# Performance work log

Hardware: AMD Instinct MI355X
Metric: run time of the kernel (lower is better)

Reference implementation:

```python
import jax, jax.numpy as jnp
import numpy as np


def setup_inputs() -> dict:
    key = jax.random.key(0)
    k1, k2, k3 = jax.random.split(key, 3)
    N, E, D_IN, D_OUT = 100000, 1600000, 64, 64
    x = jax.random.normal(k1, (N, D_IN), dtype=jnp.float32)
    edge_index = jax.random.randint(k2, (2, E), 0, N, dtype=jnp.int64)
    # Glorot-style init for the GCN weight, zero bias (PyG defaults)
    W = jax.random.normal(k3, (D_IN, D_OUT), dtype=jnp.float32) * (1.0 / np.sqrt(D_IN))
    b = jnp.zeros((D_OUT,), dtype=jnp.float32)
    return {"x": x, "edge_index": edge_index, "W": W, "b": b}


def reference(x, edge_index, W, b):
    # GCNConv (PyG semantics, add_self_loops=True, normalize=True) followed by
    # Dropout (eval mode -> identity) and ReLU.
    N = x.shape[0]
    # Linear transform first (small GEMM)
    xw = x @ W  # [N, D_OUT]
    # Add self-loops
    loops = jnp.arange(N, dtype=edge_index.dtype)
    row = jnp.concatenate([edge_index[0], loops])  # source nodes
    col = jnp.concatenate([edge_index[1], loops])  # destination nodes
    # Symmetric degree normalization: deg over destination index (PyG gcn_norm)
    ones = jnp.ones(col.shape[0], dtype=xw.dtype)
    deg = jax.ops.segment_sum(ones, col, num_segments=N)
    deg_inv_sqrt = jnp.where(deg > 0, jax.lax.rsqrt(deg), 0.0)
    norm = deg_inv_sqrt[row] * deg_inv_sqrt[col]  # [E+N]
    # Gather source features, scale, scatter-add to destinations
    msgs = norm[:, None] * xw[row]  # [E+N, D_OUT]
    out = jax.ops.segment_sum(msgs, col, num_segments=N)
    out = out + b
    # dropout in eval mode is identity
    return jax.nn.relu(out)
```

## Files before the change

### kernel.cpp

```cpp
#include <hip/hip_runtime.h>
#include <hip/hip_fp16.h>


#define D 64
#define BW 256
#define CAP 6144
#define EPT 16
#define PART_T 256
#define EPB (PART_T * EPT)

typedef __attribute__((ext_vector_type(8))) short bf16x8;
typedef __attribute__((ext_vector_type(4))) float f32x4;

__device__ __forceinline__ unsigned short f2bf(float f) {
    unsigned u = __float_as_uint(f);
    u += 0x7FFFu + ((u >> 16) & 1u);
    return (unsigned short)(u >> 16);
}

__global__ void k_part(const int* __restrict__ row, const int* __restrict__ col,
                       int* __restrict__ gcur, int* __restrict__ packed,
                       int E, int NBUCK) {
    extern __shared__ int sh[];
    int* lh   = sh;
    int* base = sh + NBUCK;
    for (int i = threadIdx.x; i < NBUCK; i += PART_T) lh[i] = 0;
    __syncthreads();
    int e0 = blockIdx.x * EPB + threadIdx.x;
    int rr[EPT], cc[EPT], pp[EPT];
#pragma unroll
    for (int i = 0; i < EPT; ++i) {
        int e = e0 + i * PART_T;
        if (e < E) {
            cc[i] = col[e];
            rr[i] = row[e];
            pp[i] = atomicAdd(&lh[cc[i] >> 8], 1);
        } else {
            cc[i] = -1;
        }
    }
    __syncthreads();
    int rot = (int)((blockIdx.x * 97u) % (unsigned)NBUCK);
    for (int j = threadIdx.x; j < NBUCK; j += PART_T) {
        int bu = j + rot; if (bu >= NBUCK) bu -= NBUCK;
        int h = lh[bu];
        if (h > 0) base[bu] = atomicAdd(&gcur[bu * 32], h);
    }
    __syncthreads();
#pragma unroll
    for (int i = 0; i < EPT; ++i) {
        if (cc[i] >= 0) {
            int bu = cc[i] >> 8;
            int pos = base[bu] + pp[i];
            if (pos < CAP)
                packed[(size_t)bu * CAP + pos] = (rr[i] << 8) | (cc[i] & 255);
        }
    }
}

__global__ void k_dis(const int* __restrict__ gcur, const int* __restrict__ packed,
                      float* __restrict__ dis, int N) {
    __shared__ int lh[BW];
    int b = blockIdx.x;
    lh[threadIdx.x] = 0;
    __syncthreads();
    int sz = min(gcur[b * 32], CAP);
    const int* pk = packed + (size_t)b * CAP;
    for (int i = threadIdx.x; i < sz; i += BW)
        atomicAdd(&lh[pk[i] & 255], 1);
    __syncthreads();
    int n = b * BW + threadIdx.x;
    if (n < N) dis[n] = rsqrtf((float)(lh[threadIdx.x] + 1));
}

__global__ __launch_bounds__(256, 4)
void k_gemm_mfma(const float* __restrict__ x, const float* __restrict__ W,
                 const float* __restrict__ dis, unsigned short* __restrict__ xw_h,
                 int N) {
    __shared__ float Ws[64 * 64];
    int tid = threadIdx.x;
    for (int i = tid; i < 4096; i += 256) Ws[i] = W[i];
    __syncthreads();
    int lane = tid & 63, wv = tid >> 6;
    int m = lane & 15, quad = lane >> 4;
    bf16x8 Bf[4][2];
#pragma unroll
    for (int t = 0; t < 4; ++t)
#pragma unroll
        for (int s = 0; s < 2; ++s) {
            bf16x8 f;
#pragma unroll
            for (int j = 0; j < 8; ++j)
                f[j] = (short)f2bf(Ws[(s * 32 + quad * 8 + j) * 64 + t * 16 + m]);
            Bf[t][s] = f;
        }
    int mt = blockIdx.x * 4 + wv;
    int row0 = mt * 16;
    if (row0 >= N) return;
    const float* xr = x + (size_t)(row0 + m) * 64 + quad * 8;
    float4 a0 = *(const float4*)(xr);
    float4 a1 = *(const float4*)(xr + 4);
    float4 a2 = *(const float4*)(xr + 32);
    float4 a3 = *(const float4*)(xr + 36);
    bf16x8 A0, A1;
    A0[0] = (short)f2bf(a0.x); A0[1] = (short)f2bf(a0.y);
    A0[2] = (short)f2bf(a0.z); A0[3] = (short)f2bf(a0.w);
    A0[4] = (short)f2bf(a1.x); A0[5] = (short)f2bf(a1.y);
    A0[6] = (short)f2bf(a1.z); A0[7] = (short)f2bf(a1.w);
    A1[0] = (short)f2bf(a2.x); A1[1] = (short)f2bf(a2.y);
    A1[2] = (short)f2bf(a2.z); A1[3] = (short)f2bf(a2.w);
    A1[4] = (short)f2bf(a3.x); A1[5] = (short)f2bf(a3.y);
    A1[6] = (short)f2bf(a3.z); A1[7] = (short)f2bf(a3.w);
    f32x4 acc[4];
#pragma unroll
    for (int t = 0; t < 4; ++t) {
        acc[t] = (f32x4){0.f, 0.f, 0.f, 0.f};
        acc[t] = __builtin_amdgcn_mfma_f32_16x16x32_bf16(A0, Bf[t][0], acc[t], 0, 0, 0);
        acc[t] = __builtin_amdgcn_mfma_f32_16x16x32_bf16(A1, Bf[t][1], acc[t], 0, 0, 0);
    }
    float4 dv = *(const float4*)(dis + row0 + quad * 4);
    float dsc[4] = {dv.x, dv.y, dv.z, dv.w};
#pragma unroll
    for (int t = 0; t < 4; ++t)
#pragma unroll
        for (int r = 0; r < 4; ++r) {
            int grow = row0 + quad * 4 + r;
            int gcol = t * 16 + m;
            xw_h[(size_t)grow * 64 + gcol] =
                __half_as_ushort(__float2half(acc[t][r] * dsc[r]));
        }
}

__global__ __launch_bounds__(1024, 8)
void k_gather(const int* __restrict__ gcur, const int* __restrict__ packed,
              const uint2* __restrict__ xwh, const float* __restrict__ bias,
              float4* __restrict__ out4, int N) {
    __shared__ int lh[BW], stt[BW], cur[BW];
    __shared__ int srtL[CAP];
    __shared__ int wsum[4];
    int b = blockIdx.x;
    int tid = threadIdx.x;
    if (tid < BW) lh[tid] = 0;
    __syncthreads();
    int sz = min(gcur[b * 32], CAP);
    const int* pk = packed + (size_t)b * CAP;
    for (int i = tid; i < sz; i += 1024)
        atomicAdd(&lh[pk[i] & 255], 1);
    __syncthreads();
    int lane = tid & 63, wv4 = tid >> 6;
    int v = (tid < BW) ? lh[tid] : 0;
    int s = v;
#pragma unroll
    for (int off = 1; off < 64; off <<= 1) {
        int u = __shfl_up(s, off);
        if (lane >= off) s += u;
    }
    if (tid < BW && lane == 63) wsum[wv4] = s;
    __syncthreads();
    if (tid < BW) {
        int woff = 0;
        for (int w = 0; w < 4; ++w) woff += (w < wv4) ? wsum[w] : 0;
        int st = woff + s - v;
        stt[tid] = st;
        cur[tid] = st;
    }
    __syncthreads();
    for (int i = tid; i < sz; i += 1024) {
        int p = pk[i];
        int pos = atomicAdd(&cur[p & 255], 1);
        srtL[pos] = p >> 8;
    }
    __syncthreads();
    int wv = tid >> 6;
    int q = lane >> 4;
    int l = lane & 15;
    const float4 bb = ((const float4*)bias)[l];
#define ADDV(h)                                                     \
    {                                                               \
        __half2 h0 = *(__half2*)&(h).x, h1 = *(__half2*)&(h).y;     \
        float2 f0 = __half22float2(h0), f1 = __half22float2(h1);    \
        acc.x += f0.x; acc.y += f0.y; acc.z += f1.x; acc.w += f1.y; \
    }
    for (int nn = wv * 16; nn < wv * 16 + 16; ++nn) {
        int node = b * BW + nn;
        if (node >= N) break;
        int k = lh[nn], s0 = stt[nn];
        float4 acc = make_float4(0.f, 0.f, 0.f, 0.f);
        if (q == 0) { uint2 hs = xwh[(size_t)node * 16 + l]; ADDV(hs); }
        int j = q;
        for (; j + 12 < k; j += 16) {
            int r0 = srtL[s0 + j];
            int r1 = srtL[s0 + j + 4];
            int r2 = srtL[s0 + j + 8];
            int r3 = srtL[s0 + j + 12];
            uint2 va = xwh[(size_t)r0 * 16 + l];
            uint2 vb = xwh[(size_t)r1 * 16 + l];
            uint2 vc = xwh[(size_t)r2 * 16 + l];
            uint2 vd = xwh[(size_t)r3 * 16 + l];
            ADDV(va); ADDV(vb); ADDV(vc); ADDV(vd);
        }
        for (; j < k; j += 4) { uint2 ve = xwh[(size_t)srtL[s0 + j] * 16 + l]; ADDV(ve); }
#pragma unroll
        for (int mm = 16; mm < 64; mm <<= 1) {
            acc.x += __shfl_xor(acc.x, mm);
            acc.y += __shfl_xor(acc.y, mm);
            acc.z += __shfl_xor(acc.z, mm);
            acc.w += __shfl_xor(acc.w, mm);
        }
        if (q == 0) {
            float dn = rsqrtf((float)(k + 1));
            float4 o;
            o.x = fmaxf(fmaf(dn, acc.x, bb.x), 0.f);
            o.y = fmaxf(fmaf(dn, acc.y, bb.y), 0.f);
            o.z = fmaxf(fmaf(dn, acc.z, bb.z), 0.f);
            o.w = fmaxf(fmaf(dn, acc.w, bb.w), 0.f);
            out4[(size_t)node * 16 + l] = o;
        }
    }
#undef ADDV
}

extern "C" void kernel_launch(void* const* d_in, const int* in_sizes, int n_in,
                              void* d_out, int out_size, void* d_ws, size_t ws_size,
                              hipStream_t stream) {
    const float* x    = (const float*)d_in[0];
    const int*   ei   = (const int*)d_in[1];
    const float* W    = (const float*)d_in[2];
    const float* bias = (const float*)d_in[3];
    float* out = (float*)d_out;

    const int N = in_sizes[0] / D;
    const int E = in_sizes[1] / 2;
    const int* row = ei;
    const int* col = ei + E;

    const int NBUCK = (N + BW - 1) / BW;
    const int NB1   = (E + EPB - 1) / EPB;
    const int NT    = (N + 15) / 16;

    char* ws = (char*)d_ws;
    size_t off = 0;
    unsigned short* xw_h = (unsigned short*)(ws + off); off += (size_t)N * D * sizeof(unsigned short);
    int* packed   = (int*)(ws + off);     off += (size_t)NBUCK * CAP * sizeof(int);
    int* gcur     = (int*)(ws + off);     off += (size_t)NBUCK * 32 * sizeof(int);
    float* dis    = (float*)(ws + off);   off += (size_t)N * sizeof(float);

    size_t ldsPart = 2u * (size_t)NBUCK * sizeof(int);

    hipMemsetAsync(gcur, 0, (size_t)NBUCK * 32 * sizeof(int), stream);
    k_part<<<NB1, PART_T, ldsPart, stream>>>(row, col, gcur, packed, E, NBUCK);
    k_dis<<<NBUCK, BW, 0, stream>>>(gcur, packed, dis, N);
    k_gemm_mfma<<<(NT + 3) / 4, 256, 0, stream>>>(x, W, dis, xw_h, N);
    k_gather<<<NBUCK, 1024, 0, stream>>>(gcur, packed, (const uint2*)xw_h, bias,
                                         (float4*)out, N);
}
```

Before: 160.2 us.

## Merge degree counting into partition, sort-coalesce scatter, and restructure gather

```diff
diff --git a/kernel.cpp b/kernel.cpp
--- a/kernel.cpp
+++ b/kernel.cpp
@@ -3,11 +3,13 @@
 
 
 #define D 64
-#define BW 256
-#define CAP 6144
+#define BW 128
+#define CAP 3072
+#define CAPP 3456
 #define EPT 16
 #define PART_T 256
 #define EPB (PART_T * EPT)
+#define NBMAX 1024
 
 typedef __attribute__((ext_vector_type(8))) short bf16x8;
 typedef __attribute__((ext_vector_type(4))) float f32x4;
@@ -18,15 +20,19 @@
     return (unsigned short)(u >> 16);
 }
 
-__global__ void k_part(const int* __restrict__ row, const int* __restrict__ col,
-                       int* __restrict__ gcur, int* __restrict__ packed,
-                       int E, int NBUCK) {
-    extern __shared__ int sh[];
-    int* lh   = sh;
-    int* base = sh + NBUCK;
-    for (int i = threadIdx.x; i < NBUCK; i += PART_T) lh[i] = 0;
-    __syncthreads();
-    int e0 = blockIdx.x * EPB + threadIdx.x;
+__global__ __launch_bounds__(256)
+void k_part(const int* __restrict__ row, const int* __restrict__ col,
+            int* __restrict__ gcur, int* __restrict__ packed,
+            int* __restrict__ deg, unsigned short* __restrict__ WT,
+            const float* __restrict__ W, unsigned short* __restrict__ xw_h,
+            int E, int NBUCK, int N) {
+    __shared__ int lh[NBMAX], base[NBMAX], lst[NBMAX];
+    __shared__ int wsc[4];
+    __shared__ int srtv[EPB], srta[EPB];
+    int tid = threadIdx.x;
+    for (int i = tid; i < NBUCK; i += PART_T) lh[i] = 0;
+    __syncthreads();
+    int e0 = blockIdx.x * EPB + tid;
     int rr[EPT], cc[EPT], pp[EPT];
 #pragma unroll
     for (int i = 0; i < EPT; ++i) {
@@ -34,146 +40,164 @@
         if (e < E) {
             cc[i] = col[e];
             rr[i] = row[e];
-            pp[i] = atomicAdd(&lh[cc[i] >> 8], 1);
+            pp[i] = atomicAdd(&lh[cc[i] >> 7], 1);
+            atomicAdd(&deg[cc[i]], 1);
         } else {
             cc[i] = -1;
         }
     }
     __syncthreads();
     int rot = (int)((blockIdx.x * 97u) % (unsigned)NBUCK);
-    for (int j = threadIdx.x; j < NBUCK; j += PART_T) {
+    for (int j = tid; j < NBUCK; j += PART_T) {
         int bu = j + rot; if (bu >= NBUCK) bu -= NBUCK;
         int h = lh[bu];
-        if (h > 0) base[bu] = atomicAdd(&gcur[bu * 32], h);
-    }
+        if (h > 0) base[bu] = atomicAdd(&gcur[bu * 8], h);
+    }
+    int lane = tid & 63, wv = tid >> 6;
+    int i0 = tid * 4;
+    int v0 = (i0     < NBUCK) ? lh[i0]     : 0;
+    int v1 = (i0 + 1 < NBUCK) ? lh[i0 + 1] : 0;
+    int v2 = (i0 + 2 < NBUCK) ? lh[i0 + 2] : 0;
+    int v3 = (i0 + 3 < NBUCK) ? lh[i0 + 3] : 0;
+    int s4 = v0 + v1 + v2 + v3, inc = s4;
+#pragma unroll
+    for (int off = 1; off < 64; off <<= 1) {
+        int u = __shfl_up(inc, off);
+        if (lane >= off) inc += u;
+    }
+    if (lane == 63) wsc[wv] = inc;
+    __syncthreads();
+    int woff = 0;
+#pragma unroll
+    for (int w = 0; w < 4; ++w) woff += (w < wv) ? wsc[w] : 0;
+    int ex = woff + inc - s4;
+    if (i0     < NBUCK) lst[i0]     = ex;
+    if (i0 + 1 < NBUCK) lst[i0 + 1] = ex + v0;
+    if (i0 + 2 < NBUCK) lst[i0 + 2] = ex + v0 + v1;
+    if (i0 + 3 < NBUCK) lst[i0 + 3] = ex + v0 + v1 + v2;
     __syncthreads();
 #pragma unroll
     for (int i = 0; i < EPT; ++i) {
         if (cc[i] >= 0) {
-            int bu = cc[i] >> 8;
-            int pos = base[bu] + pp[i];
-            if (pos < CAP)
-                packed[(size_t)bu * CAP + pos] = (rr[i] << 8) | (cc[i] & 255);
-        }
-    }
-}
-
-__global__ void k_dis(const int* __restrict__ gcur, const int* __restrict__ packed,
-                      float* __restrict__ dis, int N) {
-    __shared__ int lh[BW];
-    int b = blockIdx.x;
-    lh[threadIdx.x] = 0;
-    __syncthreads();
-    int sz = min(gcur[b * 32], CAP);
-    const int* pk = packed + (size_t)b * CAP;
-    for (int i = threadIdx.x; i < sz; i += BW)
-        atomicAdd(&lh[pk[i] & 255], 1);
-    __syncthreads();
-    int n = b * BW + threadIdx.x;
-    if (n < N) dis[n] = rsqrtf((float)(lh[threadIdx.x] + 1));
+            int bu = cc[i] >> 7;
+            int p = lst[bu] + pp[i];
+            srtv[p] = (rr[i] << 7) | (cc[i] & 127);
+            int g = base[bu] + pp[i];
+            srta[p] = (g < CAP) ? bu * CAP + g : -1;
+        }
+    }
+    __syncthreads();
+    int tot = min(EPB, E - blockIdx.x * EPB);
+    for (int p = tid; p < tot; p += PART_T) {
+        int a = srta[p];
+        if (a >= 0) packed[a] = srtv[p];
+    }
+    if (blockIdx.x == 0) {
+        for (int i = tid; i < 4096; i += PART_T) {
+            int n = i >> 6, k = i & 63;
+            WT[i] = f2bf(W[k * 64 + n]);
+        }
+        if (tid < 32) ((unsigned*)xw_h)[(size_t)N * 32 + tid] = 0u;
+    }
 }
 
 __global__ __launch_bounds__(256, 4)
-void k_gemm_mfma(const float* __restrict__ x, const float* __restrict__ W,
-                 const float* __restrict__ dis, unsigned short* __restrict__ xw_h,
-                 int N) {
-    __shared__ float Ws[64 * 64];
-    int tid = threadIdx.x;
-    for (int i = tid; i < 4096; i += 256) Ws[i] = W[i];
-    __syncthreads();
-    int lane = tid & 63, wv = tid >> 6;
+void k_gemm(const float* __restrict__ x, const unsigned short* __restrict__ WT,
+            const int* __restrict__ deg, unsigned short* __restrict__ xw_h,
+            int N, int NT, int TOTW) {
+    int tid = threadIdx.x, lane = tid & 63, wv = tid >> 6;
     int m = lane & 15, quad = lane >> 4;
     bf16x8 Bf[4][2];
 #pragma unroll
     for (int t = 0; t < 4; ++t)
 #pragma unroll
-        for (int s = 0; s < 2; ++s) {
-            bf16x8 f;
-#pragma unroll
-            for (int j = 0; j < 8; ++j)
-                f[j] = (short)f2bf(Ws[(s * 32 + quad * 8 + j) * 64 + t * 16 + m]);
-            Bf[t][s] = f;
-        }
-    int mt = blockIdx.x * 4 + wv;
-    int row0 = mt * 16;
-    if (row0 >= N) return;
-    const float* xr = x + (size_t)(row0 + m) * 64 + quad * 8;
-    float4 a0 = *(const float4*)(xr);
-    float4 a1 = *(const float4*)(xr + 4);
-    float4 a2 = *(const float4*)(xr + 32);
-    float4 a3 = *(const float4*)(xr + 36);
-    bf16x8 A0, A1;
-    A0[0] = (short)f2bf(a0.x); A0[1] = (short)f2bf(a0.y);
-    A0[2] = (short)f2bf(a0.z); A0[3] = (short)f2bf(a0.w);
-    A0[4] = (short)f2bf(a1.x); A0[5] = (short)f2bf(a1.y);
-    A0[6] = (short)f2bf(a1.z); A0[7] = (short)f2bf(a1.w);
-    A1[0] = (short)f2bf(a2.x); A1[1] = (short)f2bf(a2.y);
-    A1[2] = (short)f2bf(a2.z); A1[3] = (short)f2bf(a2.w);
-    A1[4] = (short)f2bf(a3.x); A1[5] = (short)f2bf(a3.y);
-    A1[6] = (short)f2bf(a3.z); A1[7] = (short)f2bf(a3.w);
-    f32x4 acc[4];
-#pragma unroll
-    for (int t = 0; t < 4; ++t) {
-        acc[t] = (f32x4){0.f, 0.f, 0.f, 0.f};
-        acc[t] = __builtin_amdgcn_mfma_f32_16x16x32_bf16(A0, Bf[t][0], acc[t], 0, 0, 0);
-        acc[t] = __builtin_amdgcn_mfma_f32_16x16x32_bf16(A1, Bf[t][1], acc[t], 0, 0, 0);
-    }
-    float4 dv = *(const float4*)(dis + row0 + quad * 4);
-    float dsc[4] = {dv.x, dv.y, dv.z, dv.w};
-#pragma unroll
-    for (int t = 0; t < 4; ++t)
-#pragma unroll
-        for (int r = 0; r < 4; ++r) {
-            int grow = row0 + quad * 4 + r;
-            int gcol = t * 16 + m;
-            xw_h[(size_t)grow * 64 + gcol] =
-                __half_as_ushort(__float2half(acc[t][r] * dsc[r]));
-        }
-}
-
-__global__ __launch_bounds__(1024, 8)
+        for (int s = 0; s < 2; ++s)
+            Bf[t][s] = *(const bf16x8*)(WT + (t * 16 + m) * 64 + s * 32 + quad * 8);
+    int wid = blockIdx.x * 4 + wv;
+    for (int mt = wid; mt < NT; mt += TOTW) {
+        int row0 = mt * 16;
+        const float* xr = x + (size_t)(row0 + m) * 64 + quad * 8;
+        float4 a0 = *(const float4*)(xr);
+        float4 a1 = *(const float4*)(xr + 4);
+        float4 a2 = *(const float4*)(xr + 32);
+        float4 a3 = *(const float4*)(xr + 36);
+        bf16x8 A0, A1;
+        A0[0] = (short)f2bf(a0.x); A0[1] = (short)f2bf(a0.y);
+        A0[2] = (short)f2bf(a0.z); A0[3] = (short)f2bf(a0.w);
+        A0[4] = (short)f2bf(a1.x); A0[5] = (short)f2bf(a1.y);
+        A0[6] = (short)f2bf(a1.z); A0[7] = (short)f2bf(a1.w);
+        A1[0] = (short)f2bf(a2.x); A1[1] = (short)f2bf(a2.y);
+        A1[2] = (short)f2bf(a2.z); A1[3] = (short)f2bf(a2.w);
+        A1[4] = (short)f2bf(a3.x); A1[5] = (short)f2bf(a3.y);
+        A1[6] = (short)f2bf(a3.z); A1[7] = (short)f2bf(a3.w);
+        f32x4 acc[4];
+#pragma unroll
+        for (int t = 0; t < 4; ++t) {
+            acc[t] = (f32x4){0.f, 0.f, 0.f, 0.f};
+            acc[t] = __builtin_amdgcn_mfma_f32_16x16x32_bf16(Bf[t][0], A0, acc[t], 0, 0, 0);
+            acc[t] = __builtin_amdgcn_mfma_f32_16x16x32_bf16(Bf[t][1], A1, acc[t], 0, 0, 0);
+        }
+        float dsc = rsqrtf((float)(deg[row0 + m] + 1));
+        unsigned short* op = xw_h + (size_t)(row0 + m) * 64 + quad * 4;
+#pragma unroll
+        for (int t = 0; t < 4; ++t) {
+            __half2 h0, h1;
+            h0.x = __float2half(acc[t][0] * dsc); h0.y = __float2half(acc[t][1] * dsc);
+            h1.x = __float2half(acc[t][2] * dsc); h1.y = __float2half(acc[t][3] * dsc);
+            uint2 u; u.x = *(unsigned*)&h0; u.y = *(unsigned*)&h1;
+            *(uint2*)(op + t * 16) = u;
+        }
+    }
+}
+
+__global__ __launch_bounds__(512, 8)
 void k_gather(const int* __restrict__ gcur, const int* __restrict__ packed,
               const uint2* __restrict__ xwh, const float* __restrict__ bias,
               float4* __restrict__ out4, int N) {
     __shared__ int lh[BW], stt[BW], cur[BW];
-    __shared__ int srtL[CAP];
-    __shared__ int wsum[4];
+    __shared__ int wsum[2];
+    __shared__ __align__(16) int srtL[CAPP];
     int b = blockIdx.x;
     int tid = threadIdx.x;
     if (tid < BW) lh[tid] = 0;
     __syncthreads();
-    int sz = min(gcur[b * 32], CAP);
+    int sz = min(gcur[b * 8], CAP);
     const int* pk = packed + (size_t)b * CAP;
-    for (int i = tid; i < sz; i += 1024)
-        atomicAdd(&lh[pk[i] & 255], 1);
-    __syncthreads();
-    int lane = tid & 63, wv4 = tid >> 6;
-    int v = (tid < BW) ? lh[tid] : 0;
-    int s = v;
-#pragma unroll
-    for (int off = 1; off < 64; off <<= 1) {
-        int u = __shfl_up(s, off);
-        if (lane >= off) s += u;
-    }
-    if (tid < BW && lane == 63) wsum[wv4] = s;
-    __syncthreads();
+    for (int i = tid; i < sz; i += 512)
+        atomicAdd(&lh[pk[i] & 127], 1);
+    __syncthreads();
+    int lane = tid & 63;
+    int v = 0, vp = 0, inc = 0;
     if (tid < BW) {
-        int woff = 0;
-        for (int w = 0; w < 4; ++w) woff += (w < wv4) ? wsum[w] : 0;
-        int st = woff + s - v;
+        v = lh[tid]; vp = (v + 3) & ~3; inc = vp;
+#pragma unroll
+        for (int off = 1; off < 64; off <<= 1) {
+            int u = __shfl_up(inc, off);
+            if (lane >= off) inc += u;
+        }
+        if (lane == 63) wsum[tid >> 6] = inc;
+    }
+    __syncthreads();
+    if (tid < BW) {
+        int st = inc - vp + ((tid >> 6) ? wsum[0] : 0);
         stt[tid] = st;
         cur[tid] = st;
     }
     __syncthreads();
-    for (int i = tid; i < sz; i += 1024) {
+    for (int i = tid; i < sz; i += 512) {
         int p = pk[i];
-        int pos = atomicAdd(&cur[p & 255], 1);
-        srtL[pos] = p >> 8;
-    }
-    __syncthreads();
+        int pos = atomicAdd(&cur[p & 127], 1);
+        srtL[pos] = p >> 7;
+    }
+    __syncthreads();
+    if (tid < BW) {
+        int e = stt[tid] + v, ep = stt[tid] + vp;
+        for (; e < ep; ++e) srtL[e] = N;
+    }
+    __syncthreads();
+    int l = lane & 15;
+    int ng = lane >> 4;
     int wv = tid >> 6;
-    int q = lane >> 4;
-    int l = lane & 15;
     const float4 bb = ((const float4*)bias)[l];
 #define ADDV(h)                                                     \
     {                                                               \
@@ -181,33 +205,34 @@
         float2 f0 = __half22float2(h0), f1 = __half22float2(h1);    \
         acc.x += f0.x; acc.y += f0.y; acc.z += f1.x; acc.w += f1.y; \
     }
-    for (int nn = wv * 16; nn < wv * 16 + 16; ++nn) {
+    for (int g = 0; g < 4; ++g) {
+        int nn = wv * 16 + g * 4 + ng;
         int node = b * BW + nn;
-        if (node >= N) break;
-        int k = lh[nn], s0 = stt[nn];
+        bool active = node < N;
         float4 acc = make_float4(0.f, 0.f, 0.f, 0.f);
-        if (q == 0) { uint2 hs = xwh[(size_t)node * 16 + l]; ADDV(hs); }
-        int j = q;
-        for (; j + 12 < k; j += 16) {
-            int r0 = srtL[s0 + j];
-            int r1 = srtL[s0 + j + 4];
-            int r2 = srtL[s0 + j + 8];
-            int r3 = srtL[s0 + j + 12];
-            uint2 va = xwh[(size_t)r0 * 16 + l];
-            uint2 vb = xwh[(size_t)r1 * 16 + l];
-            uint2 vc = xwh[(size_t)r2 * 16 + l];
-            uint2 vd = xwh[(size_t)r3 * 16 + l];
-            ADDV(va); ADDV(vb); ADDV(vc); ADDV(vd);
-        }
-        for (; j < k; j += 4) { uint2 ve = xwh[(size_t)srtL[s0 + j] * 16 + l]; ADDV(ve); }
-#pragma unroll
-        for (int mm = 16; mm < 64; mm <<= 1) {
-            acc.x += __shfl_xor(acc.x, mm);
-            acc.y += __shfl_xor(acc.y, mm);
-            acc.z += __shfl_xor(acc.z, mm);
-            acc.w += __shfl_xor(acc.w, mm);
-        }
-        if (q == 0) {
+        int k = 0, s0 = 0;
+        if (active) {
+            k = lh[nn]; s0 = stt[nn];
+            uint2 hs = xwh[(size_t)node * 16 + l];
+            ADDV(hs);
+        }
+        int kp = (k + 3) & ~3;
+        if (kp > 0) {
+            int4 rv = *(const int4*)&srtL[s0];
+            int j = 0;
+            while (true) {
+                uint2 va = xwh[(size_t)rv.x * 16 + l];
+                uint2 vb = xwh[(size_t)rv.y * 16 + l];
+                uint2 vc = xwh[(size_t)rv.z * 16 + l];
+                uint2 vd = xwh[(size_t)rv.w * 16 + l];
+                j += 4;
+                bool more = j < kp;
+                if (more) rv = *(const int4*)&srtL[s0 + j];
+                ADDV(va); ADDV(vb); ADDV(vc); ADDV(vd);
+                if (!more) break;
+            }
+        }
+        if (active) {
             float dn = rsqrtf((float)(k + 1));
             float4 o;
             o.x = fmaxf(fmaf(dn, acc.x, bb.x), 0.f);
@@ -237,20 +262,21 @@
     const int NBUCK = (N + BW - 1) / BW;
     const int NB1   = (E + EPB - 1) / EPB;
     const int NT    = (N + 15) / 16;
+    const int GG    = (NT + 7) / 8;
 
     char* ws = (char*)d_ws;
     size_t off = 0;
-    unsigned short* xw_h = (unsigned short*)(ws + off); off += (size_t)N * D * sizeof(unsigned short);
-    int* packed   = (int*)(ws + off);     off += (size_t)NBUCK * CAP * sizeof(int);
-    int* gcur     = (int*)(ws + off);     off += (size_t)NBUCK * 32 * sizeof(int);
-    float* dis    = (float*)(ws + off);   off += (size_t)N * sizeof(float);
-
-    size_t ldsPart = 2u * (size_t)NBUCK * sizeof(int);
-
-    hipMemsetAsync(gcur, 0, (size_t)NBUCK * 32 * sizeof(int), stream);
-    k_part<<<NB1, PART_T, ldsPart, stream>>>(row, col, gcur, packed, E, NBUCK);
-    k_dis<<<NBUCK, BW, 0, stream>>>(gcur, packed, dis, N);
-    k_gemm_mfma<<<(NT + 3) / 4, 256, 0, stream>>>(x, W, dis, xw_h, N);
-    k_gather<<<NBUCK, 1024, 0, stream>>>(gcur, packed, (const uint2*)xw_h, bias,
-                                         (float4*)out, N);
-}
+    unsigned short* xw_h = (unsigned short*)(ws + off);
+    off += (size_t)(N + 1) * D * sizeof(unsigned short);
+    int* packed = (int*)(ws + off); off += (size_t)NBUCK * CAP * sizeof(int);
+    int* gcur   = (int*)(ws + off); off += (size_t)NBUCK * 8 * sizeof(int);
+    int* deg    = (int*)(ws + off); off += (size_t)N * sizeof(int);
+    off = (off + 15) & ~(size_t)15;
+    unsigned short* WT = (unsigned short*)(ws + off); off += 4096 * sizeof(unsigned short);
+
+    hipMemsetAsync(gcur, 0, (size_t)NBUCK * 8 * sizeof(int) + (size_t)N * sizeof(int), stream);
+    k_part<<<NB1, PART_T, 0, stream>>>(row, col, gcur, packed, deg, WT, W, xw_h, E, NBUCK, N);
+    k_gemm<<<GG, 256, 0, stream>>>(x, WT, deg, xw_h, N, NT, GG * 4);
+    k_gather<<<NBUCK, 512, 0, stream>>>(gcur, packed, (const uint2*)xw_h, bias,
+                                        (float4*)out, N);
+}
```

After: 210.6 us. 1.31x slower.
